# Optimization experiments

Measured on AMD Instinct MI355X. Metric: run time of the kernel, lower is better.

Reference implementation:

```python
import jax, jax.numpy as jnp
import numpy as np

SCOPE = 27
RICKER_WIDTH = 6.0
DAMPING = 0.12
IN_CHANNELS = 256


def _ricker(scope, std, damping):
    # mexican-hat / ricker wavelet, length `scope`, centered
    x = jnp.arange(scope, dtype=jnp.float32) - (scope // 2)
    a = 2.0 / (jnp.sqrt(3.0 * std) * jnp.pi ** 0.25)
    return damping * a * (1.0 - (x / std) ** 2) * jnp.exp(-(x ** 2) / (2.0 * std ** 2))


def _pad_roll(k, in_channels):
    # zero-pad kernel (length scope) to in_channels, roll so center sits at i=0-ish
    scope = k.shape[-1]
    pad_left = (in_channels - scope) // 2
    pad_right = in_channels - scope - pad_left
    padded = jnp.concatenate([jnp.zeros((pad_left,), k.dtype), k, jnp.zeros((pad_right,), k.dtype)])
    return jnp.roll(padded, in_channels // 2 + 1)


def _circulant(kernel, c):
    # tpl[i, j] = kernel[(j - i) mod C]  (each row is the kernel rolled by i)
    idx = (jnp.arange(c)[None, :] - jnp.arange(c)[:, None]) % c
    return kernel[idx]


def setup_inputs() -> dict:
    key = jax.random.key(0)
    k1, _ = jax.random.split(key)
    activations = jax.random.normal(k1, (32, IN_CHANNELS, 64, 64), dtype=jnp.float32)
    inhibition_filter = _ricker(SCOPE, RICKER_WIDTH, DAMPING)  # learned param, ricker init
    return {"activations": activations, "inhibition_filter": inhibition_filter}


def reference(activations, inhibition_filter):
    n, c, h, w = activations.shape
    kernel = _pad_roll(inhibition_filter, c)              # [C]
    tpl = _circulant(kernel, c)                           # [C, C]
    tpl_inv = jnp.linalg.inv(jnp.eye(c, dtype=tpl.dtype) - tpl)  # [C, C]
    # torch: (N, H*W, C) @ tpl_inv -> out[n, c_out, h, w] = sum_k act[n, k, h, w] * tpl_inv[k, c_out]
    return jnp.einsum('nkhw,kc->nchw', activations, tpl_inv)
```

## Files before the change

kernel.cpp:

```cpp
#include <hip/hip_runtime.h>

#define C 256
#define HW 4096
#define STRIDE 66
#define CHROWS 32
#define NCHUNK 8
#define NBUF 4

typedef __attribute__((ext_vector_type(8))) short short8;
typedef __attribute__((ext_vector_type(4))) float float4v;

__device__ __forceinline__ unsigned short f2bf(float x) {
    unsigned u = __builtin_bit_cast(unsigned, x);
    u = (u + 0x7fffu + ((u >> 16) & 1u)) >> 16;
    return (unsigned short)u;
}

__device__ __forceinline__ void g2l_b32(const void* g, void* l) {
    __builtin_amdgcn_global_load_lds(
        (const __attribute__((address_space(1))) unsigned int*)g,
        (__attribute__((address_space(3))) unsigned int*)l, 4, 0, 0);
}
__device__ __forceinline__ void g2l_b128(const void* g, void* l) {
    __builtin_amdgcn_global_load_lds(
        (const __attribute__((address_space(1))) unsigned int*)g,
        (__attribute__((address_space(3))) unsigned int*)l, 16, 0, 0);
}

template <int N>
__device__ __forceinline__ void wait_vmcnt() {
    asm volatile("s_waitcnt vmcnt(%0)" :: "n"(N) : "memory");
    __builtin_amdgcn_sched_barrier(0);
}

__global__ void build_tab_kernel(const float* __restrict__ filt, unsigned short* __restrict__ tab) {
    __shared__ float twc[256], tws[256];
    __shared__ float Gre[256], Gim[256];
    __shared__ float gsh[256];
    const int t = threadIdx.x;
    const double PI = 3.14159265358979323846;
    double th = (double)t * (PI / 128.0);
    twc[t] = (float)cos(th);
    tws[t] = (float)sin(th);
    __syncthreads();
    float re = 1.0f, im = 0.0f;
    for (int i = 0; i < 27; ++i) {
        int d = (243 + i) & 255;
        int idx = (t * d) & 255;
        float fv = filt[i];
        re -= fv * twc[idx];
        im += fv * tws[idx];
    }
    float den = re * re + im * im;
    Gre[t] = re / den;
    Gim[t] = -im / den;
    __syncthreads();
    float acc = 0.0f;
    for (int f = 0; f < 256; ++f) {
        int idx = (f * t) & 255;
        acc += Gre[f] * twc[idx] - Gim[f] * tws[idx];
    }
    gsh[t] = acc * (1.0f / 256.0f);
    __syncthreads();
    for (int e = t; e < 16 * 64 * 8; e += 256) {
        int j = e & 7;
        int lane = (e >> 3) & 63;
        int s = e >> 9;
        int mm = lane & 15, q = lane >> 4;
        int src = (mm - 16 * s - 8 * q - j) & 255;
        tab[e] = f2bf(gsh[src]);
    }
}

__global__ __launch_bounds__(256, 3)
void toeplitz_gemm_kernel(const float* __restrict__ act,
                          const unsigned short* __restrict__ tab,
                          float* __restrict__ out) {
    __shared__ float chunkbuf[NBUF][CHROWS * STRIDE];
    __shared__ unsigned short afrags[16 * 64 * 8];

    const int tid = threadIdx.x;
    const int wave = tid >> 6;
    const int lane = tid & 63;
    const int m = lane & 15;
    const int quad = lane >> 4;
    const int blk = blockIdx.x;
    const int n = blk >> 6;
    const int p0 = (blk & 63) << 6;
    const float* __restrict__ actn = act + (size_t)n * (C * HW);
    float* __restrict__ outn = out + (size_t)n * (C * HW);

#pragma unroll
    for (int i = 0; i < 4; ++i) {
        const int seg = wave * 4 + i;
        g2l_b128(tab + seg * 512 + lane * 8, &afrags[seg * 512]);
    }

    auto issue = [&](int ch) {
        const float* src = actn + (size_t)(ch * CHROWS + wave * 8) * HW + p0 + lane;
#pragma unroll
        for (int i = 0; i < 8; ++i)
            g2l_b32(src + (size_t)i * HW, &chunkbuf[ch & (NBUF - 1)][(wave * 8 + i) * STRIDE]);
    };

    issue(0); issue(1); issue(2);

    float4v acc[4][4];
#pragma unroll
    for (int ct = 0; ct < 4; ++ct)
#pragma unroll
        for (int pt = 0; pt < 4; ++pt)
            acc[ct][pt] = (float4v){0.f, 0.f, 0.f, 0.f};

#define PHASE(c, WN)                                                              \
    {                                                                             \
        wait_vmcnt<WN>();                                                         \
        __builtin_amdgcn_s_barrier();                                             \
        __builtin_amdgcn_sched_barrier(0);                                        \
        asm volatile("" ::: "memory");                                            \
        if ((c) + 3 < NCHUNK) issue((c) + 3);                                     \
        const float* cb = &chunkbuf[(c) & (NBUF - 1)][0];                         \
        short8 bfr[4];                                                            \
        _Pragma("unroll")                                                         \
        for (int pt = 0; pt < 4; ++pt) {                                          \
            const float* base = cb + (quad * 8) * STRIDE + pt * 16 + m;           \
            unsigned u[8];                                                        \
            _Pragma("unroll")                                                     \
            for (int j = 0; j < 8; ++j)                                           \
                u[j] = __builtin_bit_cast(unsigned, base[j * STRIDE]) + 0x8000u;  \
            uint4 pk;                                                             \
            pk.x = (u[0] >> 16) | (u[1] & 0xFFFF0000u);                           \
            pk.y = (u[2] >> 16) | (u[3] & 0xFFFF0000u);                           \
            pk.z = (u[4] >> 16) | (u[5] & 0xFFFF0000u);                           \
            pk.w = (u[6] >> 16) | (u[7] & 0xFFFF0000u);                           \
            bfr[pt] = __builtin_bit_cast(short8, pk);                             \
        }                                                                         \
        _Pragma("unroll")                                                         \
        for (int ct = 0; ct < 4; ++ct) {                                          \
            const int sp = (2 * (c) - ct - 4 * wave) & 15;                        \
            const short8 af = *(const short8*)&afrags[sp * 512 + lane * 8];       \
            _Pragma("unroll")                                                     \
            for (int pt = 0; pt < 4; ++pt)                                        \
                acc[ct][pt] = __builtin_amdgcn_mfma_f32_16x16x32_bf16(            \
                    af, bfr[pt], acc[ct][pt], 0, 0, 0);                           \
        }                                                                         \
    }

    PHASE(0, 16)
    PHASE(1, 16)
    PHASE(2, 16)
    PHASE(3, 16)
    PHASE(4, 16)
    PHASE(5, 16)
    PHASE(6, 8)
    PHASE(7, 0)
#undef PHASE

#pragma unroll
    for (int ct = 0; ct < 4; ++ct) {
#pragma unroll
        for (int r = 0; r < 4; ++r) {
            const int cc = wave * 64 + ct * 16 + quad * 4 + r;
            float* op = outn + (size_t)cc * HW + p0;
#pragma unroll
            for (int pt = 0; pt < 4; ++pt) {
                op[pt * 16 + m] = acc[ct][pt][r];
            }
        }
    }
}

extern "C" void kernel_launch(void* const* d_in, const int* in_sizes, int n_in,
                              void* d_out, int out_size, void* d_ws, size_t ws_size,
                              hipStream_t stream) {
    const float* act = (const float*)d_in[0];
    const float* filt = (const float*)d_in[1];
    float* out = (float*)d_out;
    unsigned short* tab = (unsigned short*)d_ws;

    build_tab_kernel<<<1, 256, 0, stream>>>(filt, tab);
    toeplitz_gemm_kernel<<<2048, 256, 0, stream>>>(act, tab, out);
}
```

Before: 250.7 us.

## Stage activation tiles through registers with 128-bit loads and double-buffered LDS

Replaces the per-dword direct global-to-LDS loads and the four-deep LDS ring with 128-bit vector global loads into registers. Data is prefetched three chunks ahead and then written to a two-slot LDS double buffer, synchronised by an lgkmcnt wait and a barrier. The smaller LDS footprint allows the launch bound to rise from 3 to 4 blocks per CU. The goal is fewer, wider memory instructions and more latency hiding. In exchange it uses more registers for staging and adds an LDS write step per chunk.

```diff
diff --git a/kernel.cpp b/kernel.cpp
--- a/kernel.cpp
+++ b/kernel.cpp
@@ -3,9 +3,7 @@
 #define C 256
 #define HW 4096
 #define STRIDE 66
-#define CHROWS 32
 #define NCHUNK 8
-#define NBUF 4
 
 typedef __attribute__((ext_vector_type(8))) short short8;
 typedef __attribute__((ext_vector_type(4))) float float4v;
@@ -16,21 +14,10 @@
     return (unsigned short)u;
 }
 
-__device__ __forceinline__ void g2l_b32(const void* g, void* l) {
-    __builtin_amdgcn_global_load_lds(
-        (const __attribute__((address_space(1))) unsigned int*)g,
-        (__attribute__((address_space(3))) unsigned int*)l, 4, 0, 0);
-}
 __device__ __forceinline__ void g2l_b128(const void* g, void* l) {
     __builtin_amdgcn_global_load_lds(
         (const __attribute__((address_space(1))) unsigned int*)g,
         (__attribute__((address_space(3))) unsigned int*)l, 16, 0, 0);
-}
-
-template <int N>
-__device__ __forceinline__ void wait_vmcnt() {
-    asm volatile("s_waitcnt vmcnt(%0)" :: "n"(N) : "memory");
-    __builtin_amdgcn_sched_barrier(0);
 }
 
 __global__ void build_tab_kernel(const float* __restrict__ filt, unsigned short* __restrict__ tab) {
@@ -72,11 +59,11 @@
     }
 }
 
-__global__ __launch_bounds__(256, 3)
+__global__ __launch_bounds__(256, 4)
 void toeplitz_gemm_kernel(const float* __restrict__ act,
                           const unsigned short* __restrict__ tab,
                           float* __restrict__ out) {
-    __shared__ float chunkbuf[NBUF][CHROWS * STRIDE];
+    __shared__ float chunkbuf[2][32 * STRIDE];
     __shared__ unsigned short afrags[16 * 64 * 8];
 
     const int tid = threadIdx.x;
@@ -84,6 +71,7 @@
     const int lane = tid & 63;
     const int m = lane & 15;
     const int quad = lane >> 4;
+    const int pxd = (lane & 15) << 2;
     const int blk = blockIdx.x;
     const int n = blk >> 6;
     const int p0 = (blk & 63) << 6;
@@ -95,15 +83,42 @@
         const int seg = wave * 4 + i;
         g2l_b128(tab + seg * 512 + lane * 8, &afrags[seg * 512]);
     }
+    asm volatile("" ::: "memory");
 
-    auto issue = [&](int ch) {
-        const float* src = actn + (size_t)(ch * CHROWS + wave * 8) * HW + p0 + lane;
-#pragma unroll
-        for (int i = 0; i < 8; ++i)
-            g2l_b32(src + (size_t)i * HW, &chunkbuf[ch & (NBUF - 1)][(wave * 8 + i) * STRIDE]);
-    };
+    const float* __restrict__ srcp = actn + (size_t)(wave * 8) * HW + p0 + pxd;
 
-    issue(0); issue(1); issue(2);
+    uint4 sA[3], sB[3];
+
+#define RL(c)                                                                     \
+    {                                                                             \
+        sA[(c) % 3] = *(const uint4*)(srcp + (size_t)((c) * 32 + quad) * HW);     \
+        sB[(c) % 3] = *(const uint4*)(srcp + (size_t)((c) * 32 + 4 + quad) * HW); \
+    }
+#define WR(c)                                                                     \
+    {                                                                             \
+        float* dst = &chunkbuf[(c) & 1][(wave * 8 + quad) * STRIDE + pxd];        \
+        uint2 t0, t1, t2, t3;                                                     \
+        t0.x = sA[(c) % 3].x; t0.y = sA[(c) % 3].y;                               \
+        t1.x = sA[(c) % 3].z; t1.y = sA[(c) % 3].w;                               \
+        t2.x = sB[(c) % 3].x; t2.y = sB[(c) % 3].y;                               \
+        t3.x = sB[(c) % 3].z; t3.y = sB[(c) % 3].w;                               \
+        *(uint2*)(dst) = t0;                                                      \
+        *(uint2*)(dst + 2) = t1;                                                  \
+        *(uint2*)(dst + 4 * STRIDE) = t2;                                         \
+        *(uint2*)(dst + 4 * STRIDE + 2) = t3;                                     \
+    }
+#define BARRIER()                                                                 \
+    {                                                                             \
+        asm volatile("s_waitcnt lgkmcnt(0)" ::: "memory");                        \
+        __builtin_amdgcn_s_barrier();                                             \
+        asm volatile("" ::: "memory");                                            \
+    }
+
+    RL(0) RL(1) RL(2)
+    asm volatile("s_waitcnt vmcnt(6)" ::: "memory");
+    __builtin_amdgcn_sched_barrier(0);
+    WR(0)
+    BARRIER()
 
     float4v acc[4][4];
 #pragma unroll
@@ -112,14 +127,9 @@
         for (int pt = 0; pt < 4; ++pt)
             acc[ct][pt] = (float4v){0.f, 0.f, 0.f, 0.f};
 
-#define PHASE(c, WN)                                                              \
+#define COMPUTE(c)                                                                \
     {                                                                             \
-        wait_vmcnt<WN>();                                                         \
-        __builtin_amdgcn_s_barrier();                                             \
-        __builtin_amdgcn_sched_barrier(0);                                        \
-        asm volatile("" ::: "memory");                                            \
-        if ((c) + 3 < NCHUNK) issue((c) + 3);                                     \
-        const float* cb = &chunkbuf[(c) & (NBUF - 1)][0];                         \
+        const float* cb = &chunkbuf[(c) & 1][0];                                  \
         short8 bfr[4];                                                            \
         _Pragma("unroll")                                                         \
         for (int pt = 0; pt < 4; ++pt) {                                          \
@@ -146,15 +156,21 @@
         }                                                                         \
     }
 
-    PHASE(0, 16)
-    PHASE(1, 16)
-    PHASE(2, 16)
-    PHASE(3, 16)
-    PHASE(4, 16)
-    PHASE(5, 16)
-    PHASE(6, 8)
-    PHASE(7, 0)
+#define PHASE(c)                                                                  \
+    {                                                                             \
+        if ((c) + 3 < NCHUNK) RL((c) + 3)                                         \
+        if ((c) + 1 < NCHUNK) WR((c) + 1)                                         \
+        COMPUTE(c)                                                                \
+        if ((c) < NCHUNK - 1) BARRIER()                                           \
+    }
+
+    PHASE(0) PHASE(1) PHASE(2) PHASE(3)
+    PHASE(4) PHASE(5) PHASE(6) PHASE(7)
 #undef PHASE
+#undef COMPUTE
+#undef BARRIER
+#undef WR
+#undef RL
 
 #pragma unroll
     for (int ct = 0; ct < 4; ++ct) {
```

Result: slower. 261.4 us (+4.2%).

## Replace per-fragment A table with compact circulant word tables to cut LDS

Applied to the files above, without the earlier changes.

The expanded 16KB bf16 A-fragment table in LDS is replaced by two small tables of about 132 words each. They hold the circulant kernel as packed bf16 pairs at even and odd offsets, and each lane gathers its 8-element A fragment with four dword LDS reads. Launch bounds rise from 3 to 4 blocks per CU, since LDS use per block drops from roughly 50KB to about 35KB. The cost is four scalar LDS reads plus address arithmetic per fragment instead of one 128-bit read, and higher occupancy may also put pressure on registers.

```diff
diff --git a/kernel.cpp b/kernel.cpp
--- a/kernel.cpp
+++ b/kernel.cpp
@@ -21,11 +21,6 @@
         (const __attribute__((address_space(1))) unsigned int*)g,
         (__attribute__((address_space(3))) unsigned int*)l, 4, 0, 0);
 }
-__device__ __forceinline__ void g2l_b128(const void* g, void* l) {
-    __builtin_amdgcn_global_load_lds(
-        (const __attribute__((address_space(1))) unsigned int*)g,
-        (__attribute__((address_space(3))) unsigned int*)l, 16, 0, 0);
-}
 
 template <int N>
 __device__ __forceinline__ void wait_vmcnt() {
@@ -33,10 +28,11 @@
     __builtin_amdgcn_sched_barrier(0);
 }
 
-__global__ void build_tab_kernel(const float* __restrict__ filt, unsigned short* __restrict__ tab) {
+__global__ void build_tab_kernel(const float* __restrict__ filt, unsigned* __restrict__ tabw) {
     __shared__ float twc[256], tws[256];
     __shared__ float Gre[256], Gim[256];
     __shared__ float gsh[256];
+    __shared__ unsigned short gb[256];
     const int t = threadIdx.x;
     const double PI = 3.14159265358979323846;
     double th = (double)t * (PI / 128.0);
@@ -61,23 +57,23 @@
         acc += Gre[f] * twc[idx] - Gim[f] * tws[idx];
     }
     gsh[t] = acc * (1.0f / 256.0f);
+    gb[t] = f2bf(gsh[t]);
     __syncthreads();
-    for (int e = t; e < 16 * 64 * 8; e += 256) {
-        int j = e & 7;
-        int lane = (e >> 3) & 63;
-        int s = e >> 9;
-        int mm = lane & 15, q = lane >> 4;
-        int src = (mm - 16 * s - 8 * q - j) & 255;
-        tab[e] = f2bf(gsh[src]);
-    }
+    if (t < 132)
+        tabw[t] = (unsigned)gb[(256 - 2 * t) & 255]
+                | ((unsigned)gb[(256 - (2 * t + 1)) & 255] << 16);
+    if (t < 131)
+        tabw[132 + t] = (unsigned)gb[(256 - (2 * t + 1)) & 255]
+                      | ((unsigned)gb[(256 - (2 * t + 2)) & 255] << 16);
 }
 
-__global__ __launch_bounds__(256, 3)
+__global__ __launch_bounds__(256, 4)
 void toeplitz_gemm_kernel(const float* __restrict__ act,
-                          const unsigned short* __restrict__ tab,
+                          const unsigned* __restrict__ tabg,
                           float* __restrict__ out) {
     __shared__ float chunkbuf[NBUF][CHROWS * STRIDE];
-    __shared__ unsigned short afrags[16 * 64 * 8];
+    __shared__ unsigned tabA[132];
+    __shared__ unsigned tabB[132];
 
     const int tid = threadIdx.x;
     const int wave = tid >> 6;
@@ -90,11 +86,9 @@
     const float* __restrict__ actn = act + (size_t)n * (C * HW);
     float* __restrict__ outn = out + (size_t)n * (C * HW);
 
-#pragma unroll
-    for (int i = 0; i < 4; ++i) {
-        const int seg = wave * 4 + i;
-        g2l_b128(tab + seg * 512 + lane * 8, &afrags[seg * 512]);
-    }
+    if (tid < 132) tabA[tid] = tabg[tid];
+    if (tid < 131) tabB[tid] = tabg[132 + tid];
+    asm volatile("s_waitcnt lgkmcnt(0)" ::: "memory");
 
     auto issue = [&](int ch) {
         const float* src = actn + (size_t)(ch * CHROWS + wave * 8) * HW + p0 + lane;
@@ -138,7 +132,11 @@
         _Pragma("unroll")                                                         \
         for (int ct = 0; ct < 4; ++ct) {                                          \
             const int sp = (2 * (c) - ct - 4 * wave) & 15;                        \
-            const short8 af = *(const short8*)&afrags[sp * 512 + lane * 8];       \
+            const int s0 = ((sp << 4) + (quad << 3) - m) & 255;                   \
+            const unsigned* tp = ((s0 & 1) ? tabB : tabA) + (s0 >> 1);            \
+            uint4 aw;                                                             \
+            aw.x = tp[0]; aw.y = tp[1]; aw.z = tp[2]; aw.w = tp[3];               \
+            const short8 af = __builtin_bit_cast(short8, aw);                     \
             _Pragma("unroll")                                                     \
             for (int pt = 0; pt < 4; ++pt)                                        \
                 acc[ct][pt] = __builtin_amdgcn_mfma_f32_16x16x32_bf16(            \
@@ -176,8 +174,8 @@
     const float* act = (const float*)d_in[0];
     const float* filt = (const float*)d_in[1];
     float* out = (float*)d_out;
-    unsigned short* tab = (unsigned short*)d_ws;
+    unsigned* tabw = (unsigned*)d_ws;
 
-    build_tab_kernel<<<1, 256, 0, stream>>>(filt, tab);
-    toeplitz_gemm_kernel<<<2048, 256, 0, stream>>>(act, tab, out);
+    build_tab_kernel<<<1, 256, 0, stream>>>(filt, tabw);
+    toeplitz_gemm_kernel<<<2048, 256, 0, stream>>>(act, tabw, out);
 }
```

New measurement: 253.6 us. About the same (+1.2%).
